# Optimization experiments

Hardware: AMD Instinct MI355X
Metric: run time of the kernel (lower is better)

## Reference

```python
import jax, jax.numpy as jnp
import numpy as np

B, N, K = 4, 2048, 32
H, DS, DE = 128, 128, 128
NUM_IN = DS + DE + H  # 384
SCALE = 30.0
EPS = 1e-5


def setup_inputs() -> dict:
    key = jax.random.key(0)
    ks = jax.random.split(key, 9)
    s = 0.05
    return {
        "h_S": jax.random.normal(ks[0], (B, N, DS), jnp.float32),
        "h_V": jax.random.normal(ks[1], (B, N, H), jnp.float32),
        "h_E": jax.random.normal(ks[2], (B, N, K, DE), jnp.float32),
        "E_idx": jax.random.randint(ks[3], (B, N, K), 0, N, jnp.int64),
        "mask_attend": jnp.ones((B, N, K), jnp.float32),
        "W1_w": jax.random.normal(ks[4], (H + NUM_IN, H), jnp.float32) * s,
        "W1_b": jnp.zeros((H,), jnp.float32),
        "W2_w": jax.random.normal(ks[5], (H, H), jnp.float32) * s,
        "W2_b": jnp.zeros((H,), jnp.float32),
        "ln_g": jnp.ones((H,), jnp.float32),
        "ln_b": jnp.zeros((H,), jnp.float32),
    }


def gather_nodes(nodes, idx):
    # nodes: [B, N, D], idx: [B, N, K] -> [B, N, K, D]
    b, n, k = idx.shape
    d = nodes.shape[-1]
    flat = jnp.broadcast_to(idx.reshape(b, n * k, 1), (b, n * k, d))
    return jnp.take_along_axis(nodes, flat, axis=1).reshape(b, n, k, d)


def layer_norm(x, g, b):
    mu = jnp.mean(x, axis=-1, keepdims=True)
    var = jnp.var(x, axis=-1, keepdims=True)
    return (x - mu) * jax.lax.rsqrt(var + EPS) * g + b


def reference(h_S, h_V, h_E, E_idx, mask_attend, W1_w, W1_b, W2_w, W2_b, ln_g, ln_b):
    # h_ES = cat(h_E, gather(h_S))  -> [B,N,K,DE+DS]
    h_ES = jnp.concatenate([h_E, gather_nodes(h_S, E_idx)], axis=-1)
    # h_EXV = cat(h_ES, gather(h_V)) -> [B,N,K,DE+DS+H], masked
    h_EXV = jnp.concatenate([h_ES, gather_nodes(h_V, E_idx)], axis=-1)
    h_EXV = mask_attend[..., None] * h_EXV
    # h_EV = cat(h_V expanded, h_EXV) -> [B,N,K,H+NUM_IN]
    h_V_exp = jnp.broadcast_to(h_V[:, :, None, :], (h_V.shape[0], h_V.shape[1], K, h_V.shape[2]))
    h_EV = jnp.concatenate([h_V_exp, h_EXV], axis=-1)
    # per-edge 2-layer MLP (exact GELU as torch.nn.GELU)
    h = jax.nn.gelu(jnp.einsum("bnkf,fh->bnkh", h_EV, W1_w) + W1_b, approximate=False)
    h_message = jnp.einsum("bnkh,hg->bnkg", h, W2_w) + W2_b
    dh = jnp.sum(h_message, axis=-2) / SCALE
    # dropout is identity in eval mode
    return layer_norm(h_V + dh, ln_g, ln_b)
```

## Files before the change

### kernel.cpp

```cpp
#include <hip/hip_runtime.h>
#include <math.h>

typedef float f32x4 __attribute__((ext_vector_type(4)));
typedef short s16x8 __attribute__((ext_vector_type(8)));
typedef unsigned u32x4 __attribute__((ext_vector_type(4)));

#define N_NODES 2048
#define KEDGE 32
#define HDIM 128

__device__ __forceinline__ short f2bf(float f){
  unsigned u = __builtin_bit_cast(unsigned, f);
  u += 0x7fffu + ((u >> 16) & 1u);
  return (short)(u >> 16);
}

__device__ __forceinline__ unsigned cvt_pk_bf16(float a, float b){
  unsigned r;
  asm("v_cvt_pk_bf16_f32 %0, %1, %2" : "=v"(r) : "v"(a), "v"(b));
  return r;
}

__device__ __forceinline__ float fast_gelu(float x){
  float t = x * (-2.3022078f - 0.1029527f * x * x);
  float e = __builtin_amdgcn_exp2f(t);
  return x * __builtin_amdgcn_rcpf(1.0f + e);
}

__device__ __forceinline__ f32x4 mfma16(s16x8 a, s16x8 b, f32x4 c){
  return __builtin_amdgcn_mfma_f32_16x16x32_bf16(a, b, c, 0, 0, 0);
}

__global__ void prep1(const float* __restrict__ W1, const float* __restrict__ W2,
                      short* __restrict__ W1f, short* __restrict__ W2f,
                      unsigned* __restrict__ flag){
  if (blockIdx.x == 320){
    if (threadIdx.x == 0) *flag = 0u;
    return;
  }
  int t = blockIdx.x * 256 + threadIdx.x;
  if (t < 65536){
    int ks = t >> 12, r = t & 4095;
    int ct = r >> 9;  r &= 511;
    int lane = r >> 3, j = r & 7;
    int k = ks*32 + (lane>>4)*8 + j;
    int n = ct*16 + (lane&15);
    W1f[t] = f2bf(W1[k*128 + n]);
  } else if (t < 81920){
    int t2 = t - 65536;
    int ks = t2 >> 12, r = t2 & 4095;
    int ct = r >> 9;  r &= 511;
    int lane = r >> 3, j = r & 7;
    int k = ks*32 + (lane>>4)*8 + j;
    int n = ct*16 + (lane&15);
    W2f[t2] = f2bf(W2[k*128 + n]);
  }
}

__global__ __launch_bounds__(256)
void prep2(const float* __restrict__ hS, const float* __restrict__ hV,
           const float* __restrict__ b1, const short* __restrict__ W1f,
           float* __restrict__ Z, float* __restrict__ U,
           const unsigned* __restrict__ Ei_u, unsigned* __restrict__ flag){
  if (blockIdx.x >= 128){
    int t = ((int)blockIdx.x - 128)*256 + threadIdx.x;
    unsigned v = Ei_u[2*t + 1];
    unsigned long long m = __ballot(v != 0u);
    if ((threadIdx.x & 63) == 0 && m) atomicOr(flag, 1u);
    return;
  }
  const int tid = threadIdx.x;
  const int w = tid >> 6, lane = tid & 63, l15 = lane & 15, lg = lane >> 4;
  const int nb = ((int)blockIdx.x*4 + w)*16;

  f32x4 accz[8], accu[8];
  #pragma unroll
  for (int ct = 0; ct < 8; ++ct){ accz[ct] = (f32x4){0,0,0,0}; accu[ct] = (f32x4){0,0,0,0}; }

  #pragma unroll
  for (int ks = 0; ks < 4; ++ks){
    const float* p = hS + (long)(nb + l15)*128 + ks*32 + lg*8;
    float4 x = *(const float4*)p, y = *(const float4*)(p + 4);
    u32x4 pk;
    pk[0] = cvt_pk_bf16(x.x, x.y); pk[1] = cvt_pk_bf16(x.z, x.w);
    pk[2] = cvt_pk_bf16(y.x, y.y); pk[3] = cvt_pk_bf16(y.z, y.w);
    s16x8 a = __builtin_bit_cast(s16x8, pk);
    #pragma unroll
    for (int ct = 0; ct < 8; ++ct){
      s16x8 bf = *(const s16x8*)(W1f + (8+ks)*4096 + ct*512 + lane*8);
      accz[ct] = mfma16(a, bf, accz[ct]);
    }
  }
  #pragma unroll
  for (int ks = 0; ks < 4; ++ks){
    const float* p = hV + (long)(nb + l15)*128 + ks*32 + lg*8;
    float4 x = *(const float4*)p, y = *(const float4*)(p + 4);
    u32x4 pk;
    pk[0] = cvt_pk_bf16(x.x, x.y); pk[1] = cvt_pk_bf16(x.z, x.w);
    pk[2] = cvt_pk_bf16(y.x, y.y); pk[3] = cvt_pk_bf16(y.z, y.w);
    s16x8 a = __builtin_bit_cast(s16x8, pk);
    #pragma unroll
    for (int ct = 0; ct < 8; ++ct){
      s16x8 bfd = *(const s16x8*)(W1f + (12+ks)*4096 + ct*512 + lane*8);
      accz[ct] = mfma16(a, bfd, accz[ct]);
      s16x8 bfa = *(const s16x8*)(W1f + (0+ks)*4096 + ct*512 + lane*8);
      accu[ct] = mfma16(a, bfa, accu[ct]);
    }
  }

  float b1v[8];
  #pragma unroll
  for (int ct = 0; ct < 8; ++ct) b1v[ct] = b1[ct*16 + l15];

  #pragma unroll
  for (int ct = 0; ct < 8; ++ct)
    #pragma unroll
    for (int i = 0; i < 4; ++i){
      const long row = nb + lg*4 + i;
      Z[row*128 + ct*16 + l15] = accz[ct][i];
      U[row*128 + ct*16 + l15] = accu[ct][i] + b1v[ct];
    }
}

__global__ __launch_bounds__(256, 4)
void fusedF(const float* __restrict__ hE, const int* __restrict__ Eidx,
            const float* __restrict__ mask, const float* __restrict__ hV,
            const float* __restrict__ W2b, const float* __restrict__ lng,
            const float* __restrict__ lnb, const short* __restrict__ W1f,
            const short* __restrict__ W2f, const float* __restrict__ Z,
            const float* __restrict__ U, const unsigned* __restrict__ idx_flag,
            float* __restrict__ out)
{
  __shared__ short vbc[4][128];

  const int tid  = threadIdx.x;
  const int w    = tid >> 6;
  const int lane = tid & 63;
  const int l15  = lane & 15;
  const int lg   = lane >> 4;

  const int bid  = (int)blockIdx.x;
  const int bswz = (bid & 7)*256 + (bid >> 3);
  const int ng   = bswz*4 + w;
  const int b    = ng >> 11;
  const long nodeoff = (long)ng * HDIM;
  const int  ebase   = ng * KEDGE;

  const int is64 = (*idx_flag == 0u);
  int eidx[2]; float mval[2];
  #pragma unroll
  for (int rt = 0; rt < 2; ++rt){
    int e = ebase + rt*16 + l15;
    eidx[rt] = is64 ? Eidx[2*e] : Eidx[e];
    mval[rt] = mask[e];
  }

  float uv[8];
  #pragma unroll
  for (int ct = 0; ct < 8; ++ct) uv[ct] = U[nodeoff + ct*16 + l15];

  s16x8 ifr[2];
  #pragma unroll
  for (int c2 = 0; c2 < 2; ++c2){
    const int active = ((lg >> 1) == c2);
    const int j = l15 - 8*(lg & 1);
    s16x8 f;
    #pragma unroll
    for (int e = 0; e < 8; ++e)
      f[e] = (active && j == e) ? (short)0x3F80 : (short)0;
    ifr[c2] = f;
  }

  f32x4 acc1[2][8];
  #pragma unroll
  for (int rt = 0; rt < 2; ++rt)
    #pragma unroll
    for (int ct = 0; ct < 8; ++ct) acc1[rt][ct] = (f32x4){0,0,0,0};

  const short* Wb = W1f + 16384;

  float4 ecur[2][2], enxt[2][2];
  #pragma unroll
  for (int rt = 0; rt < 2; ++rt){
    const float* p = hE + (long)(ebase + rt*16 + l15)*128 + lg*8;
    ecur[rt][0] = *(const float4*)p;
    ecur[rt][1] = *(const float4*)(p + 4);
  }

  #pragma unroll
  for (int ks = 0; ks < 4; ++ks){
    if (ks < 3){
      #pragma unroll
      for (int rt = 0; rt < 2; ++rt){
        const float* p = hE + (long)(ebase + rt*16 + l15)*128 + (ks+1)*32 + lg*8;
        enxt[rt][0] = *(const float4*)p;
        enxt[rt][1] = *(const float4*)(p + 4);
      }
    }
    float4 zr[2][2];
    #pragma unroll
    for (int rt = 0; rt < 2; ++rt){
      const float* zp = Z + (long)(b*N_NODES + eidx[rt])*128 + ks*32 + lg*8;
      zr[rt][0] = *(const float4*)zp;
      zr[rt][1] = *(const float4*)(zp + 4);
    }
    s16x8 a[2];
    #pragma unroll
    for (int rt = 0; rt < 2; ++rt){
      float4 x = ecur[rt][0], y = ecur[rt][1];
      float sc = mval[rt];
      u32x4 pk;
      pk[0] = cvt_pk_bf16(x.x*sc, x.y*sc); pk[1] = cvt_pk_bf16(x.z*sc, x.w*sc);
      pk[2] = cvt_pk_bf16(y.x*sc, y.y*sc); pk[3] = cvt_pk_bf16(y.z*sc, y.w*sc);
      a[rt] = __builtin_bit_cast(s16x8, pk);
    }
    const short* bb = Wb + ks*4096 + lane*8;
    #pragma unroll
    for (int ct = 0; ct < 8; ++ct){
      s16x8 bf = *(const s16x8*)(bb + ct*512);
      acc1[0][ct] = mfma16(a[0], bf, acc1[0][ct]);
      acc1[1][ct] = mfma16(a[1], bf, acc1[1][ct]);
    }
    s16x8 az[2];
    #pragma unroll
    for (int rt = 0; rt < 2; ++rt){
      float4 x = zr[rt][0], y = zr[rt][1];
      float sc = mval[rt];
      u32x4 pk;
      pk[0] = cvt_pk_bf16(x.x*sc, x.y*sc); pk[1] = cvt_pk_bf16(x.z*sc, x.w*sc);
      pk[2] = cvt_pk_bf16(y.x*sc, y.y*sc); pk[3] = cvt_pk_bf16(y.z*sc, y.w*sc);
      az[rt] = __builtin_bit_cast(s16x8, pk);
    }
    #pragma unroll
    for (int c2 = 0; c2 < 2; ++c2){
      const int ct = ks*2 + c2;
      acc1[0][ct] = mfma16(az[0], ifr[c2], acc1[0][ct]);
      acc1[1][ct] = mfma16(az[1], ifr[c2], acc1[1][ct]);
    }
    if (ks < 3){
      #pragma unroll
      for (int rt = 0; rt < 2; ++rt){
        ecur[rt][0] = enxt[rt][0]; ecur[rt][1] = enxt[rt][1];
      }
    }
  }

  float v8[8];
  #pragma unroll
  for (int ct = 0; ct < 8; ++ct){
    float s = 0.f;
    #pragma unroll
    for (int rt = 0; rt < 2; ++rt)
      #pragma unroll
      for (int i = 0; i < 4; ++i)
        s += fast_gelu(acc1[rt][ct][i] + uv[ct]);
    s += __shfl_xor(s, 16, 64);
    s += __shfl_xor(s, 32, 64);
    v8[ct] = s;
  }

  short* vl = &vbc[w][0];
  #pragma unroll
  for (int q = 0; q < 2; ++q){
    const int ct = lg*2 + q;
    vl[ct*16 + l15] = f2bf(v8[ct]);
  }
  asm volatile("s_waitcnt lgkmcnt(0)" ::: "memory");
  __builtin_amdgcn_sched_barrier(0);

  f32x4 acc2[8];
  #pragma unroll
  for (int ct = 0; ct < 8; ++ct) acc2[ct] = (f32x4){0,0,0,0};

  s16x8 av[4];
  #pragma unroll
  for (int ks2 = 0; ks2 < 4; ++ks2)
    av[ks2] = *(const s16x8*)(vl + ks2*32 + lg*8);

  #pragma unroll
  for (int ks2 = 0; ks2 < 4; ++ks2){
    const short* wb = W2f + ks2*4096 + lane*8;
    #pragma unroll
    for (int ct = 0; ct < 8; ++ct){
      s16x8 bf = *(const s16x8*)(wb + ct*512);
      acc2[ct] = mfma16(av[ks2], bf, acc2[ct]);
    }
  }

  float res[8];
  float vs = 0.f, vq = 0.f;
  #pragma unroll
  for (int ct = 0; ct < 8; ++ct){
    const int c = ct*16 + l15;
    float dh  = (acc2[ct][0] + 32.0f * W2b[c]) * (1.0f/30.0f);
    float val = hV[nodeoff + c] + dh;
    res[ct] = val;
    vs += val; vq += val*val;
  }
  vs += __shfl_xor(vs, 1, 64);  vs += __shfl_xor(vs, 2, 64);
  vs += __shfl_xor(vs, 4, 64);  vs += __shfl_xor(vs, 8, 64);
  vq += __shfl_xor(vq, 1, 64);  vq += __shfl_xor(vq, 2, 64);
  vq += __shfl_xor(vq, 4, 64);  vq += __shfl_xor(vq, 8, 64);
  const float mu  = vs * (1.0f/128.0f);
  const float var = vq * (1.0f/128.0f) - mu*mu;
  const float rs  = rsqrtf(var + 1e-5f);

  #pragma unroll
  for (int q = 0; q < 2; ++q){
    const int ct = lg*2 + q;
    const int c  = ct*16 + l15;
    out[nodeoff + c] = (res[ct] - mu) * rs * lng[c] + lnb[c];
  }
}

extern "C" void kernel_launch(void* const* d_in, const int* in_sizes, int n_in,
                              void* d_out, int out_size, void* d_ws, size_t ws_size,
                              hipStream_t stream) {
  const float* hS  = (const float*)d_in[0];
  const float* hV  = (const float*)d_in[1];
  const float* hE  = (const float*)d_in[2];
  const int*   Ei  = (const int*)d_in[3];
  const float* mk  = (const float*)d_in[4];
  const float* W1w = (const float*)d_in[5];
  const float* W1b = (const float*)d_in[6];
  const float* W2w = (const float*)d_in[7];
  const float* W2b = (const float*)d_in[8];
  const float* lng = (const float*)d_in[9];
  const float* lnb = (const float*)d_in[10];

  short* W1f = (short*)d_ws;
  short* W2f = W1f + 65536;
  unsigned* flag = (unsigned*)((char*)d_ws + 163840);
  float* Z = (float*)((char*)d_ws + 164096);
  float* U = Z + 1048576;

  prep1<<<321, 256, 0, stream>>>(W1w, W2w, W1f, W2f, flag);
  prep2<<<640, 256, 0, stream>>>(hS, hV, W1b, W1f, Z, U, (const unsigned*)Ei, flag);
  fusedF<<<2048, 256, 0, stream>>>(hE, Ei, mk, hV, W2b, lng, lnb,
                                   W1f, W2f, Z, U, flag, (float*)d_out);
}
```

Measured before the change: 92.97 us.

## Stage edge and gathered rows in LDS via direct global-to-LDS loads, split node across two waves

```diff
diff --git a/kernel.cpp b/kernel.cpp
--- a/kernel.cpp
+++ b/kernel.cpp
@@ -25,6 +25,12 @@
   float t = x * (-2.3022078f - 0.1029527f * x * x);
   float e = __builtin_amdgcn_exp2f(t);
   return x * __builtin_amdgcn_rcpf(1.0f + e);
+}
+
+__device__ __forceinline__ void gld16(const void* g, void* l){
+  __builtin_amdgcn_global_load_lds(
+      (const __attribute__((address_space(1))) void*)g,
+      (__attribute__((address_space(3))) void*)l, 16, 0, 0);
 }
 
 __device__ __forceinline__ f32x4 mfma16(s16x8 a, s16x8 b, f32x4 c){
@@ -122,7 +128,7 @@
     }
 }
 
-__global__ __launch_bounds__(256, 4)
+__global__ __launch_bounds__(256, 2)
 void fusedF(const float* __restrict__ hE, const int* __restrict__ Eidx,
             const float* __restrict__ mask, const float* __restrict__ hV,
             const float* __restrict__ W2b, const float* __restrict__ lng,
@@ -131,33 +137,52 @@
             const float* __restrict__ U, const unsigned* __restrict__ idx_flag,
             float* __restrict__ out)
 {
-  __shared__ short vbc[4][128];
+  __shared__ __align__(16) char smem[67584];
 
   const int tid  = threadIdx.x;
   const int w    = tid >> 6;
   const int lane = tid & 63;
   const int l15  = lane & 15;
   const int lg   = lane >> 4;
+  const int h    = w & 1;
 
   const int bid  = (int)blockIdx.x;
-  const int bswz = (bid & 7)*256 + (bid >> 3);
-  const int ng   = bswz*4 + w;
+  const int bswz = (bid & 7)*512 + (bid >> 3);
+  const int ng   = bswz*2 + (w >> 1);
   const int b    = ng >> 11;
   const long nodeoff = (long)ng * HDIM;
   const int  ebase   = ng * KEDGE;
 
+  char* wbase = smem + w*16384;
+  const int rr = lane >> 5;
+  const int g  = lane & 31;
+
+  #pragma unroll
+  for (int q = 0; q < 8; ++q){
+    const int r = 2*q + rr;
+    const float* src = hE + (((long)(ebase + h*16 + r)) << 7) + ((g ^ (r & 6)) << 2);
+    gld16(src, wbase + q*1024);
+  }
+
   const int is64 = (*idx_flag == 0u);
-  int eidx[2]; float mval[2];
-  #pragma unroll
-  for (int rt = 0; rt < 2; ++rt){
-    int e = ebase + rt*16 + l15;
-    eidx[rt] = is64 ? Eidx[2*e] : Eidx[e];
-    mval[rt] = mask[e];
-  }
-
-  float uv[8];
-  #pragma unroll
-  for (int ct = 0; ct < 8; ++ct) uv[ct] = U[nodeoff + ct*16 + l15];
+  const int er   = ebase + h*16 + l15;
+  const int eidx = is64 ? Eidx[2*er] : Eidx[er];
+  const float mval = mask[er];
+
+  #pragma unroll
+  for (int q = 0; q < 8; ++q){
+    const int r = 2*q + rr;
+    const int e_r = __shfl(eidx, 2*q + rr, 64);
+    const float* src = Z + (((long)(b*N_NODES + e_r)) << 7) + ((g ^ (r & 6)) << 2);
+    gld16(src, wbase + 8192 + q*1024);
+  }
+
+  float uv[8], hvv[8];
+  #pragma unroll
+  for (int ct = 0; ct < 8; ++ct){
+    uv[ct]  = U[nodeoff + ct*16 + l15];
+    hvv[ct] = hV[nodeoff + ct*16 + l15];
+  }
 
   s16x8 ifr[2];
   #pragma unroll
@@ -171,78 +196,43 @@
     ifr[c2] = f;
   }
 
-  f32x4 acc1[2][8];
-  #pragma unroll
-  for (int rt = 0; rt < 2; ++rt)
-    #pragma unroll
-    for (int ct = 0; ct < 8; ++ct) acc1[rt][ct] = (f32x4){0,0,0,0};
+  asm volatile("s_waitcnt vmcnt(0)" ::: "memory");
+  __builtin_amdgcn_sched_barrier(0);
+
+  f32x4 acc1[8];
+  #pragma unroll
+  for (int ct = 0; ct < 8; ++ct) acc1[ct] = (f32x4){0,0,0,0};
 
   const short* Wb = W1f + 16384;
 
-  float4 ecur[2][2], enxt[2][2];
-  #pragma unroll
-  for (int rt = 0; rt < 2; ++rt){
-    const float* p = hE + (long)(ebase + rt*16 + l15)*128 + lg*8;
-    ecur[rt][0] = *(const float4*)p;
-    ecur[rt][1] = *(const float4*)(p + 4);
-  }
-
   #pragma unroll
   for (int ks = 0; ks < 4; ++ks){
-    if (ks < 3){
-      #pragma unroll
-      for (int rt = 0; rt < 2; ++rt){
-        const float* p = hE + (long)(ebase + rt*16 + l15)*128 + (ks+1)*32 + lg*8;
-        enxt[rt][0] = *(const float4*)p;
-        enxt[rt][1] = *(const float4*)(p + 4);
-      }
-    }
-    float4 zr[2][2];
-    #pragma unroll
-    for (int rt = 0; rt < 2; ++rt){
-      const float* zp = Z + (long)(b*N_NODES + eidx[rt])*128 + ks*32 + lg*8;
-      zr[rt][0] = *(const float4*)zp;
-      zr[rt][1] = *(const float4*)(zp + 4);
-    }
-    s16x8 a[2];
-    #pragma unroll
-    for (int rt = 0; rt < 2; ++rt){
-      float4 x = ecur[rt][0], y = ecur[rt][1];
-      float sc = mval[rt];
-      u32x4 pk;
-      pk[0] = cvt_pk_bf16(x.x*sc, x.y*sc); pk[1] = cvt_pk_bf16(x.z*sc, x.w*sc);
-      pk[2] = cvt_pk_bf16(y.x*sc, y.y*sc); pk[3] = cvt_pk_bf16(y.z*sc, y.w*sc);
-      a[rt] = __builtin_bit_cast(s16x8, pk);
-    }
+    const int gsw = ((ks*8 + lg*2) ^ (l15 & 6)) << 4;
+    const char* pe = wbase + l15*512 + gsw;
+    float4 ex = *(const float4*)pe;
+    float4 ey = *(const float4*)(pe + 16);
+    u32x4 pk;
+    pk[0] = cvt_pk_bf16(ex.x*mval, ex.y*mval); pk[1] = cvt_pk_bf16(ex.z*mval, ex.w*mval);
+    pk[2] = cvt_pk_bf16(ey.x*mval, ey.y*mval); pk[3] = cvt_pk_bf16(ey.z*mval, ey.w*mval);
+    s16x8 a = __builtin_bit_cast(s16x8, pk);
+
     const short* bb = Wb + ks*4096 + lane*8;
     #pragma unroll
     for (int ct = 0; ct < 8; ++ct){
       s16x8 bf = *(const s16x8*)(bb + ct*512);
-      acc1[0][ct] = mfma16(a[0], bf, acc1[0][ct]);
-      acc1[1][ct] = mfma16(a[1], bf, acc1[1][ct]);
-    }
-    s16x8 az[2];
-    #pragma unroll
-    for (int rt = 0; rt < 2; ++rt){
-      float4 x = zr[rt][0], y = zr[rt][1];
-      float sc = mval[rt];
-      u32x4 pk;
-      pk[0] = cvt_pk_bf16(x.x*sc, x.y*sc); pk[1] = cvt_pk_bf16(x.z*sc, x.w*sc);
-      pk[2] = cvt_pk_bf16(y.x*sc, y.y*sc); pk[3] = cvt_pk_bf16(y.z*sc, y.w*sc);
-      az[rt] = __builtin_bit_cast(s16x8, pk);
-    }
-    #pragma unroll
-    for (int c2 = 0; c2 < 2; ++c2){
-      const int ct = ks*2 + c2;
-      acc1[0][ct] = mfma16(az[0], ifr[c2], acc1[0][ct]);
-      acc1[1][ct] = mfma16(az[1], ifr[c2], acc1[1][ct]);
-    }
-    if (ks < 3){
-      #pragma unroll
-      for (int rt = 0; rt < 2; ++rt){
-        ecur[rt][0] = enxt[rt][0]; ecur[rt][1] = enxt[rt][1];
-      }
-    }
+      acc1[ct] = mfma16(a, bf, acc1[ct]);
+    }
+
+    const char* pz = wbase + 8192 + l15*512 + gsw;
+    float4 zx = *(const float4*)pz;
+    float4 zy = *(const float4*)(pz + 16);
+    u32x4 zk;
+    zk[0] = cvt_pk_bf16(zx.x*mval, zx.y*mval); zk[1] = cvt_pk_bf16(zx.z*mval, zx.w*mval);
+    zk[2] = cvt_pk_bf16(zy.x*mval, zy.y*mval); zk[3] = cvt_pk_bf16(zy.z*mval, zy.w*mval);
+    s16x8 az = __builtin_bit_cast(s16x8, zk);
+    #pragma unroll
+    for (int c2 = 0; c2 < 2; ++c2)
+      acc1[ks*2 + c2] = mfma16(az, ifr[c2], acc1[ks*2 + c2]);
   }
 
   float v8[8];
@@ -250,39 +240,47 @@
   for (int ct = 0; ct < 8; ++ct){
     float s = 0.f;
     #pragma unroll
-    for (int rt = 0; rt < 2; ++rt)
-      #pragma unroll
-      for (int i = 0; i < 4; ++i)
-        s += fast_gelu(acc1[rt][ct][i] + uv[ct]);
+    for (int i = 0; i < 4; ++i)
+      s += fast_gelu(acc1[ct][i] + uv[ct]);
     s += __shfl_xor(s, 16, 64);
     s += __shfl_xor(s, 32, 64);
     v8[ct] = s;
   }
 
-  short* vl = &vbc[w][0];
-  #pragma unroll
-  for (int q = 0; q < 2; ++q){
-    const int ct = lg*2 + q;
-    vl[ct*16 + l15] = f2bf(v8[ct]);
-  }
-  asm volatile("s_waitcnt lgkmcnt(0)" ::: "memory");
-  __builtin_amdgcn_sched_barrier(0);
+  float* vex = (float*)(smem + 65536) + w*128;
+  if (lg == 0){
+    #pragma unroll
+    for (int ct = 0; ct < 8; ++ct) vex[ct*16 + l15] = v8[ct];
+  }
+  __syncthreads();
+  const float* vexP = (float*)(smem + 65536) + (w^1)*128;
+
+  s16x8 av[4];
+  #pragma unroll
+  for (int ks2 = 0; ks2 < 4; ++ks2){
+    const int off = ks2*32 + lg*8;
+    float4 a0 = *(const float4*)(vex + off);
+    float4 a1 = *(const float4*)(vex + off + 4);
+    float4 b0 = *(const float4*)(vexP + off);
+    float4 b1 = *(const float4*)(vexP + off + 4);
+    u32x4 pk;
+    pk[0] = cvt_pk_bf16(a0.x+b0.x, a0.y+b0.y);
+    pk[1] = cvt_pk_bf16(a0.z+b0.z, a0.w+b0.w);
+    pk[2] = cvt_pk_bf16(a1.x+b1.x, a1.y+b1.y);
+    pk[3] = cvt_pk_bf16(a1.z+b1.z, a1.w+b1.w);
+    av[ks2] = __builtin_bit_cast(s16x8, pk);
+  }
 
   f32x4 acc2[8];
   #pragma unroll
   for (int ct = 0; ct < 8; ++ct) acc2[ct] = (f32x4){0,0,0,0};
 
-  s16x8 av[4];
-  #pragma unroll
-  for (int ks2 = 0; ks2 < 4; ++ks2)
-    av[ks2] = *(const s16x8*)(vl + ks2*32 + lg*8);
-
   #pragma unroll
   for (int ks2 = 0; ks2 < 4; ++ks2){
-    const short* wb = W2f + ks2*4096 + lane*8;
+    const short* wb2 = W2f + ks2*4096 + lane*8;
     #pragma unroll
     for (int ct = 0; ct < 8; ++ct){
-      s16x8 bf = *(const s16x8*)(wb + ct*512);
+      s16x8 bf = *(const s16x8*)(wb2 + ct*512);
       acc2[ct] = mfma16(av[ks2], bf, acc2[ct]);
     }
   }
@@ -293,7 +291,7 @@
   for (int ct = 0; ct < 8; ++ct){
     const int c = ct*16 + l15;
     float dh  = (acc2[ct][0] + 32.0f * W2b[c]) * (1.0f/30.0f);
-    float val = hV[nodeoff + c] + dh;
+    float val = hvv[ct] + dh;
     res[ct] = val;
     vs += val; vq += val*val;
   }
@@ -305,11 +303,13 @@
   const float var = vq * (1.0f/128.0f) - mu*mu;
   const float rs  = rsqrtf(var + 1e-5f);
 
-  #pragma unroll
-  for (int q = 0; q < 2; ++q){
-    const int ct = lg*2 + q;
-    const int c  = ct*16 + l15;
-    out[nodeoff + c] = (res[ct] - mu) * rs * lng[c] + lnb[c];
+  if (h == 0){
+    #pragma unroll
+    for (int q = 0; q < 2; ++q){
+      const int ct = lg*2 + q;
+      const int c  = ct*16 + l15;
+      out[nodeoff + c] = (res[ct] - mu) * rs * lng[c] + lnb[c];
+    }
   }
 }
 
@@ -336,6 +336,6 @@
 
   prep1<<<321, 256, 0, stream>>>(W1w, W2w, W1f, W2f, flag);
   prep2<<<640, 256, 0, stream>>>(hS, hV, W1b, W1f, Z, U, (const unsigned*)Ei, flag);
-  fusedF<<<2048, 256, 0, stream>>>(hE, Ei, mk, hV, W2b, lng, lnb,
+  fusedF<<<4096, 256, 0, stream>>>(hE, Ei, mk, hV, W2b, lng, lnb,
                                    W1f, W2f, Z, U, flag, (float*)d_out);
 }
```

Result: slower. 105.8 us (+13.8%).
